# Optimization experiments

Measured on AMD Instinct MI355X. Metric: run time of the kernel, lower is better.

## Reference

```python
import jax, jax.numpy as jnp
import numpy as np

D_MODEL = 1024
NUM_HEADS = 16
HEAD_DIM = D_MODEL // NUM_HEADS
FF_DIM = 4096
EPS = 1e-5


def _layer_norm(x, gamma, beta):
    mu = jnp.mean(x, axis=-1, keepdims=True)
    var = jnp.var(x, axis=-1, keepdims=True)
    return (x - mu) * jax.lax.rsqrt(var + EPS) * gamma + beta


def setup_inputs() -> dict:
    key0 = jax.random.key(0)
    ks = jax.random.split(key0, 20)
    s = 0.02
    B, S = 2, 2048
    inp = {
        'value': jax.random.normal(ks[0], (B, S, D_MODEL), jnp.float32),
        'key': jax.random.normal(ks[1], (B, S, D_MODEL), jnp.float32),
        'query': jax.random.normal(ks[2], (B, S, D_MODEL), jnp.float32),
        # attention projections (stored [in, out]; y = x @ W + b)
        'wq': jax.random.normal(ks[3], (D_MODEL, D_MODEL), jnp.float32) * s,
        'bq': jnp.zeros((D_MODEL,), jnp.float32),
        'wk': jax.random.normal(ks[4], (D_MODEL, D_MODEL), jnp.float32) * s,
        'bk': jnp.zeros((D_MODEL,), jnp.float32),
        'wv': jax.random.normal(ks[5], (D_MODEL, D_MODEL), jnp.float32) * s,
        'bv': jnp.zeros((D_MODEL,), jnp.float32),
        'wo': jax.random.normal(ks[6], (D_MODEL, D_MODEL), jnp.float32) * s,
        'bo': jnp.zeros((D_MODEL,), jnp.float32),
        # layernorm 1
        'g1': jnp.ones((D_MODEL,), jnp.float32),
        'beta1': jnp.zeros((D_MODEL,), jnp.float32),
        # feed-forward
        'w1': jax.random.normal(ks[7], (D_MODEL, FF_DIM), jnp.float32) * s,
        'b1': jnp.zeros((FF_DIM,), jnp.float32),
        'w2': jax.random.normal(ks[8], (FF_DIM, D_MODEL), jnp.float32) * s,
        'b2': jnp.zeros((D_MODEL,), jnp.float32),
        # layernorm 2
        'g2': jnp.ones((D_MODEL,), jnp.float32),
        'beta2': jnp.zeros((D_MODEL,), jnp.float32),
    }
    return inp


def reference(value, key, query, wq, bq, wk, bk, wv, bv, wo, bo,
              g1, beta1, w1, b1, w2, b2, g2, beta2):
    B, S, _ = query.shape
    # QKV projections -> [B, S, H, Dh]
    Q = (query @ wq + bq).reshape(B, S, NUM_HEADS, HEAD_DIM)
    K = (key @ wk + bk).reshape(B, S, NUM_HEADS, HEAD_DIM)
    V = (value @ wv + bv).reshape(B, S, NUM_HEADS, HEAD_DIM)
    # scaled dot-product attention (full score matrix, as in source)
    energy = jnp.einsum('bqhd,bkhd->bhqk', Q, K) / jnp.sqrt(jnp.float32(HEAD_DIM))
    attn = jax.nn.softmax(energy, axis=-1)
    out = jnp.einsum('bhqk,bkhd->bqhd', attn, V).reshape(B, S, D_MODEL)
    attn_out = out @ wo + bo
    # residual + norm1 (dropout is identity in eval)
    x = _layer_norm(attn_out + query, g1, beta1)
    # feed-forward
    ff = jax.nn.relu(x @ w1 + b1) @ w2 + b2
    # residual + norm2
    return _layer_norm(ff + x, g2, beta2)
```

## Files before the change

kernel.cpp:

```cpp
#include <hip/hip_runtime.h>
#include <hip/hip_bf16.h>
#include <cstdint>
#include <math.h>

typedef __bf16 bf16_t;
typedef __attribute__((ext_vector_type(2))) __bf16 bf16x2;
typedef __attribute__((ext_vector_type(4))) __bf16 bf16x4;
typedef __attribute__((ext_vector_type(8))) __bf16 bf16x8;
typedef __attribute__((ext_vector_type(4))) float f32x4;
typedef __attribute__((ext_vector_type(16))) float f32x16;
typedef __attribute__((ext_vector_type(2))) int int2v;
typedef __attribute__((ext_vector_type(4))) int int4v;

#define B_SZ 2
#define S_SZ 2048
#define D_MODEL 1024
#define NUM_HEADS 16
#define HEAD_DIM 64
#define FF_DIM 4096
#define M_ROWS (B_SZ * S_SZ)

#define CF 0.180336880f
#define THRC 2.0f

__device__ __forceinline__ float fexp2(float x) { return __builtin_amdgcn_exp2f(x); }

__device__ __forceinline__ void gload_lds16(const void* g, void* lds) {
    __builtin_amdgcn_global_load_lds(
        (const __attribute__((address_space(1))) void*)(uintptr_t)g,
        (__attribute__((address_space(3))) void*)(uint32_t)(uintptr_t)lds,
        16, 0, 0);
}

__device__ __forceinline__ f32x4 mfma16(bf16x8 a, bf16x8 b, f32x4 c) {
    return __builtin_amdgcn_mfma_f32_16x16x32_bf16(a, b, c, 0, 0, 0);
}
__device__ __forceinline__ f32x16 mfma32(bf16x8 a, bf16x8 b, f32x16 c) {
    return __builtin_amdgcn_mfma_f32_32x32x16_bf16(a, b, c, 0, 0, 0);
}
__device__ __forceinline__ int2v plswap(int a, int b) {
    return __builtin_amdgcn_permlane32_swap(a, b, false, false);
}
__device__ __forceinline__ int packbf(float a, float b) {
    bf16x2 t; t[0] = (bf16_t)a; t[1] = (bf16_t)b;
    return __builtin_bit_cast(int, t);
}

__device__ __forceinline__ int xcd_swz(int lin, int nwg) {
    return (lin & 7) * (nwg >> 3) + (lin >> 3);
}

__global__ __launch_bounds__(256) void cast3_f32_bf16(const float* __restrict__ in0,
                                                      const float* __restrict__ in1,
                                                      const float* __restrict__ in2,
                                                      bf16_t* __restrict__ out0,
                                                      bf16_t* __restrict__ out1,
                                                      bf16_t* __restrict__ out2) {
    int which = blockIdx.x >> 12;
    int blk = blockIdx.x & 4095;
    const float* in = which == 0 ? in0 : which == 1 ? in1 : in2;
    bf16_t* out = which == 0 ? out0 : which == 1 ? out1 : out2;
    size_t i = ((size_t)blk * 256 + threadIdx.x) * 4;
    float4 v = *(const float4*)(in + i);
    bf16x4 o;
    o[0] = (bf16_t)v.x; o[1] = (bf16_t)v.y; o[2] = (bf16_t)v.z; o[3] = (bf16_t)v.w;
    *(bf16x4*)(out + i) = o;
}

__global__ __launch_bounds__(256) void transpose_cast_w4(const float* __restrict__ W0,
                                                         const float* __restrict__ W1,
                                                         const float* __restrict__ W2,
                                                         const float* __restrict__ W3,
                                                         bf16_t* __restrict__ T0,
                                                         bf16_t* __restrict__ T1,
                                                         bf16_t* __restrict__ T2,
                                                         bf16_t* __restrict__ T3) {
    __shared__ float t[32][33];
    const int K = 1024, N = 1024;
    const float* W = blockIdx.z == 0 ? W0 : blockIdx.z == 1 ? W1 : blockIdx.z == 2 ? W2 : W3;
    bf16_t* WT = blockIdx.z == 0 ? T0 : blockIdx.z == 1 ? T1 : blockIdx.z == 2 ? T2 : T3;
    int tid = threadIdx.x;
    int rr = tid >> 3, cc = (tid & 7) * 4;
    int k0 = blockIdx.x * 32, n0 = blockIdx.y * 32;
    float4 v = *(const float4*)(W + (size_t)(k0 + rr) * N + n0 + cc);
    t[rr][cc + 0] = v.x; t[rr][cc + 1] = v.y; t[rr][cc + 2] = v.z; t[rr][cc + 3] = v.w;
    __syncthreads();
    bf16x4 o;
    o[0] = (bf16_t)t[cc + 0][rr]; o[1] = (bf16_t)t[cc + 1][rr];
    o[2] = (bf16_t)t[cc + 2][rr]; o[3] = (bf16_t)t[cc + 3][rr];
    *(bf16x4*)(WT + (size_t)(n0 + rr) * K + k0 + cc) = o;
}

__global__ __launch_bounds__(256) void transpose_cast_w(const float* __restrict__ W,
                                                        bf16_t* __restrict__ WT,
                                                        int K, int N) {
    __shared__ float t[32][33];
    int tid = threadIdx.x;
    int rr = tid >> 3, cc = (tid & 7) * 4;
    int k0 = blockIdx.x * 32, n0 = blockIdx.y * 32;
    float4 v = *(const float4*)(W + (size_t)(k0 + rr) * N + n0 + cc);
    t[rr][cc + 0] = v.x; t[rr][cc + 1] = v.y; t[rr][cc + 2] = v.z; t[rr][cc + 3] = v.w;
    __syncthreads();
    bf16x4 o;
    o[0] = (bf16_t)t[cc + 0][rr]; o[1] = (bf16_t)t[cc + 1][rr];
    o[2] = (bf16_t)t[cc + 2][rr]; o[3] = (bf16_t)t[cc + 3][rr];
    *(bf16x4*)(WT + (size_t)(n0 + rr) * K + k0 + cc) = o;
}

__global__ __launch_bounds__(256) void transpose_v(const bf16_t* __restrict__ Vp,
                                                   bf16_t* __restrict__ VT) {
    __shared__ bf16_t t[32][34];
    int tid = threadIdx.x;
    int rr = tid >> 3, cc = (tid & 7) * 4;
    int bh = blockIdx.z;
    int b = bh >> 4, h = bh & 15;
    int s0 = blockIdx.x * 32, d0 = blockIdx.y * 32;
    bf16x4 v = *(const bf16x4*)(Vp + ((size_t)(b * S_SZ + s0 + rr)) * D_MODEL + h * HEAD_DIM + d0 + cc);
    t[rr][cc + 0] = v[0]; t[rr][cc + 1] = v[1]; t[rr][cc + 2] = v[2]; t[rr][cc + 3] = v[3];
    __syncthreads();
    bf16x4 o;
    o[0] = t[cc + 0][rr]; o[1] = t[cc + 1][rr]; o[2] = t[cc + 2][rr]; o[3] = t[cc + 3][rr];
    *(bf16x4*)(VT + ((size_t)(bh * HEAD_DIM + d0 + rr)) * S_SZ + s0 + cc) = o;
}

template<int BNF, bool RELU, bool OUT_BF16, bool OUT_F32>
__device__ __forceinline__ void gemm8p_core(const bf16_t* __restrict__ Ag, int lda,
                                            const bf16_t* __restrict__ Bg, int ldb,
                                            const float* __restrict__ bias, bool useBias,
                                            float* __restrict__ Cf,
                                            bf16_t* __restrict__ Cb,
                                            int N, int Klen, int m0, int n0,
                                            bf16_t* sA, bf16_t* sB) {
    constexpr int BSTRIDE = (BNF == 4) ? 16384 : 8192;
    const int tid = threadIdx.x;
    const int lane = tid & 63, w = tid >> 6;
    const int g = lane >> 4, r = lane & 15;
    const int ah = w >> 2;
    const int bh = (BNF == 4) ? ((w & 3) >> 1) : 0;
    const int wbr = (BNF == 4) ? ((w & 1) * 64) : ((w & 3) * 32);
    const int rs = r & 7;

    const int scol = ((tid & 7) ^ ((tid >> 3) & 7)) * 8;
    const bf16_t* aSrc = Ag + (size_t)(m0 + (tid >> 3)) * lda + scol;
    const bf16_t* bSrc = Bg + (size_t)(n0 + (tid >> 3)) * ldb + scol;

    f32x4 acc[8][BNF];
#pragma unroll
    for (int i = 0; i < 8; i++)
#pragma unroll
        for (int j = 0; j < BNF; j++)
#pragma unroll
            for (int e = 0; e < 4; e++) acc[i][j][e] = 0.f;

    auto stageA = [&](int buf, int half, int k0) {
        const bf16_t* s = aSrc + (size_t)(half * 128) * lda + k0;
        bf16_t* d = sA + buf * 16384 + half * 8192 + tid * 8;
        gload_lds16(s, d);
        gload_lds16(s + (size_t)64 * lda, d + 4096);
    };
    auto stageB = [&](int buf, int half, int k0) {
        const bf16_t* s = bSrc + (size_t)(half * 128) * ldb + k0;
        bf16_t* d = sB + buf * BSTRIDE + half * 8192 + tid * 8;
        gload_lds16(s, d);
        gload_lds16(s + (size_t)64 * ldb, d + 4096);
    };

    bf16x8 af[4][2];
    bf16x8 bfr[BNF / 2][2];

    auto READ = [&](int buf, int ih, int jsel) {
        const bf16_t* mA = sA + buf * 16384 + ah * 8192;
        const bf16_t* mB = sB + buf * BSTRIDE + bh * 8192;
#pragma unroll
        for (int ii = 0; ii < 4; ii++) {
            const int rho = ih + ii * 16 + r;
#pragma unroll
            for (int kk = 0; kk < 2; kk++)
                af[ii][kk] = *(const bf16x8*)(mA + rho * 64 + (((kk << 2) | g) ^ rs) * 8);
        }
#pragma unroll
        for (int jj = 0; jj < BNF / 2; jj++) {
            const int rho = wbr + jsel * (BNF == 4 ? 32 : 16) + jj * 16 + r;
#pragma unroll
            for (int kk = 0; kk < 2; kk++)
                bfr[jj][kk] = *(const bf16x8*)(mB + rho * 64 + (((kk << 2) | g) ^ rs) * 8);
        }
    };
    auto QUAD = [&](int ih4, int jsel) {
        __builtin_amdgcn_s_setprio(1);
#pragma unroll
        for (int ii = 0; ii < 4; ii++)
#pragma unroll
            for (int jj = 0; jj < BNF / 2; jj++)
#pragma unroll
                for (int kk = 0; kk < 2; kk++)
                    acc[ih4 + ii][jsel * (BNF / 2) + jj] =
                        mfma16(af[ii][kk], bfr[jj][kk], acc[ih4 + ii][jsel * (BNF / 2) + jj]);
        __builtin_amdgcn_s_setprio(0);
    };

#define LGKM0() do { asm volatile("s_waitcnt lgkmcnt(0)" ::: "memory"); \
                     __builtin_amdgcn_sched_barrier(0); } while (0)

    const int nk = Klen >> 6;
    stageA(0, 0, 0); stageA(0, 1, 0); stageB(0, 0, 0);
    if constexpr (BNF == 4) stageB(0, 1, 0);

    for (int t = 0; t < nk; ++t) {
        const int buf = t & 1, nb = buf ^ 1;
        const int kn = (t + 1) << 6;
        const bool hn = (t + 1 < nk);
        if (hn) { stageA(nb, 0, kn); asm volatile("s_waitcnt vmcnt(2)" ::: "memory"); }
        else    { asm volatile("s_waitcnt vmcnt(0)" ::: "memory"); }
        __builtin_amdgcn_s_barrier();
        READ(buf, 0, 0);
        LGKM0();
        QUAD(0, 0);
        __builtin_amdgcn_s_barrier();
        READ(buf, 0, 1);
        if (hn) stageA(nb, 1, kn);
        __builtin_amdgcn_s_barrier();
        LGKM0();
        QUAD(0, 1);
        __builtin_amdgcn_s_barrier();
        READ(buf, 64, 0);
        if (hn) stageB(nb, 0, kn);
        __builtin_amdgcn_s_barrier();
        LGKM0();
        QUAD(4, 0);
        __builtin_amdgcn_s_barrier();
        READ(buf, 64, 1);
        if constexpr (BNF == 4) { if (hn) stageB(nb, 1, kn); }
        __builtin_amdgcn_s_barrier();
        LGKM0();
        QUAD(4, 1);
        __builtin_amdgcn_s_barrier();
    }
#undef LGKM0

#pragma unroll
    for (int j = 0; j < BNF; j++) {
        int n = n0 + (w & 3) * (16 * BNF) + j * 16 + r;
        float bv = useBias ? bias[n] : 0.f;
#pragma unroll
        for (int i = 0; i < 8; i++) {
#pragma unroll
            for (int rr = 0; rr < 4; rr++) {
                int mrow = m0 + (w >> 2) * 128 + i * 16 + g * 4 + rr;
                float val = acc[i][j][rr] + bv;
                if (RELU) val = fmaxf(val, 0.f);
                if (OUT_F32) Cf[(size_t)mrow * N + n] = val;
                if (OUT_BF16) Cb[(size_t)mrow * N + n] = (bf16_t)val;
            }
        }
    }
}

template<int BNF, bool RELU, bool OUT_BF16, bool OUT_F32>
__global__ __launch_bounds__(512, 1) void gemm8p(const bf16_t* __restrict__ A, int lda,
                                                 const bf16_t* __restrict__ Bt, int ldb,
                                                 const float* __restrict__ bias,
                                                 float* __restrict__ Cf0,
                                                 float* __restrict__ Cf1,
                                                 bf16_t* __restrict__ Cb,
                                                 int N, int Klen) {
    __shared__ bf16_t sA[2 * 16384];
    __shared__ bf16_t sB[2 * ((BNF == 4) ? 16384 : 8192)];
    const int lin = blockIdx.x + gridDim.x * (blockIdx.y + gridDim.y * blockIdx.z);
    const int nwg = gridDim.x * gridDim.y * gridDim.z;
    const int sz = xcd_swz(lin, nwg);
    const int bx = sz % gridDim.x;
    const int rest = sz / gridDim.x;
    const int by = rest % gridDim.y;
    const int bz = rest / gridDim.y;
    const int koff = bz * Klen;
    gemm8p_core<BNF, RELU, OUT_BF16, OUT_F32>(A + koff, lda, Bt + koff, ldb,
                                              bias, bz == 0,
                                              bz ? Cf1 : Cf0, Cb, N, Klen,
                                              bx * 256, by * (64 * BNF), sA, sB);
}

__global__ __launch_bounds__(512, 1) void gemm_qkv8p(const bf16_t* __restrict__ A0,
                                                     const bf16_t* __restrict__ A1,
                                                     const bf16_t* __restrict__ A2,
                                                     const bf16_t* __restrict__ B0,
                                                     const bf16_t* __restrict__ B1,
                                                     const bf16_t* __restrict__ B2,
                                                     const float* __restrict__ b0,
                                                     const float* __restrict__ b1,
                                                     const float* __restrict__ b2,
                                                     bf16_t* __restrict__ C0,
                                                     bf16_t* __restrict__ C1,
                                                     bf16_t* __restrict__ C2) {
    __shared__ bf16_t sA[2 * 16384];
    __shared__ bf16_t sB[2 * 16384];
    const int lin = blockIdx.x + gridDim.x * (blockIdx.y + gridDim.y * blockIdx.z);
    const int nwg = gridDim.x * gridDim.y * gridDim.z;
    const int sz = xcd_swz(lin, nwg);
    const int bx = sz % gridDim.x;
    const int rest = sz / gridDim.x;
    const int by = rest % gridDim.y;
    const int bz = rest / gridDim.y;
    const bf16_t* A = bz == 0 ? A0 : bz == 1 ? A1 : A2;
    const bf16_t* Bt = bz == 0 ? B0 : bz == 1 ? B1 : B2;
    const float* bias = bz == 0 ? b0 : bz == 1 ? b1 : b2;
    bf16_t* C = bz == 0 ? C0 : bz == 1 ? C1 : C2;
    gemm8p_core<4, false, true, false>(A, 1024, Bt, 1024, bias, true,
                                       nullptr, C, 1024, 1024, bx * 256, by * 256, sA, sB);
}

__device__ __forceinline__ void flash_tile(
    const char* kt, const char* vt, int l31, int hi,
    const bf16x8 (&bq)[4],
    f32x16& o0, f32x16& o1, float& mC, float& l_run)
{
    bf16x8 ak[4];
#pragma unroll
    for (int kb = 0; kb < 4; kb++)
        ak[kb] = *(const bf16x8*)(kt + l31 * 128 + (((kb << 1) | hi) ^ (l31 & 7)) * 16);
    bf16x8 av[4];
#pragma unroll
    for (int db = 0; db < 2; db++)
#pragma unroll
        for (int kb = 0; kb < 2; kb++)
            av[db * 2 + kb] = *(const bf16x8*)(vt + (db * 32 + l31) * 64 + ((((kb << 1) | hi)) ^ ((l31 >> 1) & 3)) * 16);

    f32x16 s;
#pragma unroll
    for (int e = 0; e < 16; e++) s[e] = 0.f;
#pragma unroll
    for (int kb = 0; kb < 4; kb++) s = mfma32(ak[kb], bq[kb], s);

    float ma = fmaxf(fmaxf(s[0], s[1]), fmaxf(s[2], s[3]));
    float mb = fmaxf(fmaxf(s[4], s[5]), fmaxf(s[6], s[7]));
    float mc = fmaxf(fmaxf(s[8], s[9]), fmaxf(s[10], s[11]));
    float md = fmaxf(fmaxf(s[12], s[13]), fmaxf(s[14], s[15]));
    float pmaxC = fmaxf(fmaxf(ma, mb), fmaxf(mc, md)) * CF;

    if (!__all(pmaxC <= mC + THRC)) {
        int2v pr = plswap(__float_as_int(pmaxC), __float_as_int(pmaxC));
        float rowmaxC = fmaxf(__int_as_float(pr[0]), __int_as_float(pr[1]));
        float mnewC = fmaxf(mC, rowmaxC);
        float alpha = fexp2(mC - mnewC);
        mC = mnewC;
        l_run *= alpha;
#pragma unroll
        for (int e = 0; e < 16; e++) { o0[e] *= alpha; o1[e] *= alpha; }
    }

#pragma unroll
    for (int e = 0; e < 16; e++) s[e] = fexp2(__builtin_fmaf(s[e], CF, -mC));
    float t0 = (s[0] + s[1]) + (s[2] + s[3]);
    float t1 = (s[4] + s[5]) + (s[6] + s[7]);
    float t2 = (s[8] + s[9]) + (s[10] + s[11]);
    float t3 = (s[12] + s[13]) + (s[14] + s[15]);
    l_run += (t0 + t1) + (t2 + t3);

#pragma unroll
    for (int kb2 = 0; kb2 < 2; kb2++) {
        const int bse = kb2 * 8;
        int W0 = packbf(s[bse + 0], s[bse + 1]);
        int W1 = packbf(s[bse + 2], s[bse + 3]);
        int W2 = packbf(s[bse + 4], s[bse + 5]);
        int W3 = packbf(s[bse + 6], s[bse + 7]);
        int2v r02 = plswap(W0, W2);
        int2v r13 = plswap(W1, W3);
        int4v fw; fw[0] = r02[0]; fw[1] = r13[0]; fw[2] = r02[1]; fw[3] = r13[1];
        bf16x8 pf = __builtin_bit_cast(bf16x8, fw);
        o0 = mfma32(av[kb2], pf, o0);
        o1 = mfma32(av[2 + kb2], pf, o1);
    }
}

__global__ __launch_bounds__(256) void flash_attn(const bf16_t* __restrict__ Qp,
                                                  const bf16_t* __restrict__ Kp,
                                                  const bf16_t* __restrict__ VT,
                                                  bf16_t* __restrict__ Oa) {
    __shared__ alignas(16) char lds[2][2][8192];
    const int tid = threadIdx.x;
    const int lane = tid & 63;
    const int wave = tid >> 6;
    const int half = wave >> 1;
    const int qt = wave & 1;
    const int l31 = lane & 31, hi = lane >> 5;

    const int lin = blockIdx.x + (blockIdx.y << 5) + (blockIdx.z << 9);
    const int swz = (lin & 7) * 128 + (lin >> 3);
    const int qb = swz & 31;
    const int h = (swz >> 5) & 15;
    const int b = swz >> 9;

    const int q0 = qb * 64 + qt * 32;

    const bf16_t* Qb = Qp + (size_t)b * S_SZ * D_MODEL + h * HEAD_DIM;
    const bf16_t* Kb = Kp + (size_t)b * S_SZ * D_MODEL + h * HEAD_DIM;
    const bf16_t* Vb = VT + ((size_t)(b * NUM_HEADS + h) * HEAD_DIM) * S_SZ;

    const int sh = wave & 1;
    const int skvbase = sh * (S_SZ / 2);
    const bool kRole = wave < 2;

    const bf16_t* src_run;
    size_t inner_stride;
    size_t tile_stride;
    char* dst0;
    char* dst1;
    if (kRole) {
        src_run = Kb + (size_t)(skvbase + (lane >> 3)) * D_MODEL + ((lane & 7) ^ (lane >> 3)) * 8;
        inner_stride = (size_t)8 * D_MODEL;
        tile_stride = (size_t)32 * D_MODEL;
        dst0 = &lds[0][sh][0] + lane * 16;
        dst1 = &lds[1][sh][0] + lane * 16;
    } else {
        src_run = Vb + (size_t)(lane >> 2) * S_SZ + skvbase + ((lane & 3) ^ ((lane >> 3) & 3)) * 8;
        inner_stride = (size_t)16 * S_SZ;
        tile_stride = 32;
        dst0 = &lds[0][sh][4096] + lane * 16;
        dst1 = &lds[1][sh][4096] + lane * 16;
    }

    bf16x8 bq[4];
#pragma unroll
    for (int kb = 0; kb < 4; kb++)
        bq[kb] = *(const bf16x8*)(Qb + (size_t)(q0 + l31) * D_MODEL + kb * 16 + hi * 8);

    f32x16 o0, o1;
#pragma unroll
    for (int e = 0; e < 16; e++) { o0[e] = 0.f; o1[e] = 0.f; }
    float mC = -1e30f, l_run = 0.f;

    const char* kt0 = &lds[0][half][0];
    const char* vt0 = &lds[0][half][4096];
    const char* kt1 = &lds[1][half][0];
    const char* vt1 = &lds[1][half][4096];

#pragma unroll
    for (int ii = 0; ii < 4; ii++)
        gload_lds16(src_run + ii * inner_stride, dst0 + ii * 1024);
    src_run += tile_stride;
    __syncthreads();

    for (int t = 0; t < 32; t += 2) {
#pragma unroll
        for (int ii = 0; ii < 4; ii++)
            gload_lds16(src_run + ii * inner_stride, dst1 + ii * 1024);
        src_run += tile_stride;
        flash_tile(kt0, vt0, l31, hi, bq, o0, o1, mC, l_run);
        __syncthreads();

        if (t + 2 < 32) {
#pragma unroll
            for (int ii = 0; ii < 4; ii++)
                gload_lds16(src_run + ii * inner_stride, dst0 + ii * 1024);
            src_run += tile_stride;
        }
        flash_tile(kt1, vt1, l31, hi, bq, o0, o1, mC, l_run);
        __syncthreads();
    }

    int2v lp = plswap(__float_as_int(l_run), __float_as_int(l_run));
    l_run = __int_as_float(lp[0]) + __int_as_float(lp[1]);

    float (*obuf)[2][64] = (float (*)[2][64])(&lds[0][0][0]);
    float (*mrg)[64][2] = (float (*)[64][2])(&lds[0][0][0] + 16384);
    if (half == 1) {
        mrg[qt][lane][0] = mC;
        mrg[qt][lane][1] = l_run;
#pragma unroll
        for (int e = 0; e < 16; e++) {
            obuf[e][qt][lane] = o0[e];
            obuf[16 + e][qt][lane] = o1[e];
        }
    }
    __syncthreads();
    if (half == 0) {
        const float m2C = mrg[qt][lane][0], l2 = mrg[qt][lane][1];
        const float mm = fmaxf(mC, m2C);
        const float e1 = fexp2(mC - mm);
        const float e2 = fexp2(m2C - mm);
        const float linv = 1.f / (l_run * e1 + l2 * e2);
        bf16_t* Orow = Oa + ((size_t)b * S_SZ + q0 + l31) * D_MODEL + h * HEAD_DIM;
#pragma unroll
        for (int db = 0; db < 2; db++) {
#pragma unroll
            for (int rq = 0; rq < 4; rq++) {
                bf16x4 st;
#pragma unroll
                for (int i = 0; i < 4; i++) {
                    const int e = rq * 4 + i;
                    const float own = db ? o1[e] : o0[e];
                    const float oth = obuf[db * 16 + e][qt][lane];
                    st[i] = (bf16_t)((own * e1 + oth * e2) * linv);
                }
                *(bf16x4*)(Orow + db * 32 + rq * 8 + hi * 4) = st;
            }
        }
    }
}

__global__ __launch_bounds__(256) void ln_fused(const float* __restrict__ A,
                                                const float* __restrict__ A2,
                                                const float* __restrict__ R,
                                                const float* __restrict__ gamma,
                                                const float* __restrict__ beta,
                                                float* __restrict__ Xf,
                                                bf16_t* __restrict__ Xb) {
    __shared__ float red[8];
    int row = blockIdx.x, tid = threadIdx.x;
    size_t base = (size_t)row * D_MODEL + tid * 4;
    float4 a = *(const float4*)(A + base);
    float4 rv = *(const float4*)(R + base);
    float v0 = a.x + rv.x, v1 = a.y + rv.y, v2 = a.z + rv.z, v3 = a.w + rv.w;
    if (A2) {
        float4 a2 = *(const float4*)(A2 + base);
        v0 += a2.x; v1 += a2.y; v2 += a2.z; v3 += a2.w;
    }
    float s = v0 + v1 + v2 + v3;
    float q = v0 * v0 + v1 * v1 + v2 * v2 + v3 * v3;
#pragma unroll
    for (int off = 32; off; off >>= 1) { s += __shfl_down(s, off); q += __shfl_down(q, off); }
    if ((tid & 63) == 0) { red[tid >> 6] = s; red[4 + (tid >> 6)] = q; }
    __syncthreads();
    s = red[0] + red[1] + red[2] + red[3];
    q = red[4] + red[5] + red[6] + red[7];
    float mean = s * (1.f / D_MODEL);
    float var = q * (1.f / D_MODEL) - mean * mean;
    float rstd = rsqrtf(var + 1e-5f);
    float4 gm = *(const float4*)(gamma + tid * 4);
    float4 bt = *(const float4*)(beta + tid * 4);
    float y0 = (v0 - mean) * rstd * gm.x + bt.x;
    float y1 = (v1 - mean) * rstd * gm.y + bt.y;
    float y2 = (v2 - mean) * rstd * gm.z + bt.z;
    float y3 = (v3 - mean) * rstd * gm.w + bt.w;
    float4 yo; yo.x = y0; yo.y = y1; yo.z = y2; yo.w = y3;
    *(float4*)(Xf + base) = yo;
    if (Xb) {
        bf16x4 ob; ob[0] = (bf16_t)y0; ob[1] = (bf16_t)y1; ob[2] = (bf16_t)y2; ob[3] = (bf16_t)y3;
        *(bf16x4*)(Xb + base) = ob;
    }
}

extern "C" void kernel_launch(void* const* d_in, const int* in_sizes, int n_in,
                              void* d_out, int out_size, void* d_ws, size_t ws_size,
                              hipStream_t stream) {
    const float* value = (const float*)d_in[0];
    const float* key   = (const float*)d_in[1];
    const float* query = (const float*)d_in[2];
    const float* wq = (const float*)d_in[3];
    const float* bq = (const float*)d_in[4];
    const float* wk = (const float*)d_in[5];
    const float* bk = (const float*)d_in[6];
    const float* wv = (const float*)d_in[7];
    const float* bv = (const float*)d_in[8];
    const float* wo = (const float*)d_in[9];
    const float* bo = (const float*)d_in[10];
    const float* g1 = (const float*)d_in[11];
    const float* beta1 = (const float*)d_in[12];
    const float* w1 = (const float*)d_in[13];
    const float* b1 = (const float*)d_in[14];
    const float* w2 = (const float*)d_in[15];
    const float* b2 = (const float*)d_in[16];
    const float* g2 = (const float*)d_in[17];
    const float* beta2 = (const float*)d_in[18];
    (void)in_sizes; (void)n_in; (void)out_size; (void)ws_size;

    const size_t MB = 1ull << 20;
    char* ws = (char*)d_ws;
    bf16_t* wqT = (bf16_t*)(ws + 0 * MB);
    bf16_t* wkT = (bf16_t*)(ws + 2 * MB);
    bf16_t* wvT = (bf16_t*)(ws + 4 * MB);
    bf16_t* woT = (bf16_t*)(ws + 6 * MB);
    bf16_t* w1T = (bf16_t*)(ws + 8 * MB);
    bf16_t* w2T = (bf16_t*)(ws + 16 * MB);
    bf16_t* q_bf = (bf16_t*)(ws + 24 * MB);
    bf16_t* k_bf = (bf16_t*)(ws + 32 * MB);
    bf16_t* v_bf = (bf16_t*)(ws + 40 * MB);
    bf16_t* Qp  = (bf16_t*)(ws + 48 * MB);
    bf16_t* Kp  = (bf16_t*)(ws + 56 * MB);
    bf16_t* Vp  = (bf16_t*)(ws + 64 * MB);
    bf16_t* VT  = (bf16_t*)(ws + 72 * MB);
    bf16_t* attn = (bf16_t*)(ws + 24 * MB);
    float*  woP0 = (float*)(ws + 32 * MB);
    float*  woP1 = (float*)(ws + 48 * MB);
    float*  x_f = (float*)(ws + 64 * MB);
    bf16_t* x_b = (bf16_t*)(ws + 24 * MB);
    bf16_t* h_b = (bf16_t*)(ws + 32 * MB);
    float*  ffP0 = (float*)(ws + 80 * MB);
    float*  ffP1 = (float*)(ws + 96 * MB);

    dim3 blk(256);
    dim3 blk512(512);

    cast3_f32_bf16<<<12288, blk, 0, stream>>>(query, key, value, q_bf, k_bf, v_bf);
    transpose_cast_w4<<<dim3(32, 32, 4), blk, 0, stream>>>(wq, wk, wv, wo, wqT, wkT, wvT, woT);
    transpose_cast_w<<<dim3(32, 128), blk, 0, stream>>>(w1, w1T, 1024, 4096);
    transpose_cast_w<<<dim3(128, 32), blk, 0, stream>>>(w2, w2T, 4096, 1024);

    gemm_qkv8p<<<dim3(16, 4, 3), blk512, 0, stream>>>(q_bf, k_bf, v_bf, wqT, wkT, wvT,
                                                      bq, bk, bv, Qp, Kp, Vp);

    transpose_v<<<dim3(64, 2, 32), blk, 0, stream>>>(Vp, VT);

    flash_attn<<<dim3(32, 16, 2), blk, 0, stream>>>(Qp, Kp, VT, attn);

    gemm8p<2, false, false, true><<<dim3(16, 8, 2), blk512, 0, stream>>>(attn, 1024, woT, 1024, bo, woP0, woP1, nullptr, D_MODEL, 512);

    ln_fused<<<4096, blk, 0, stream>>>(woP0, woP1, query, g1, beta1, x_f, x_b);

    gemm8p<4, true, true, false><<<dim3(16, 16, 1), blk512, 0, stream>>>(x_b, 1024, w1T, 1024, b1, nullptr, nullptr, h_b, FF_DIM, 1024);

    gemm8p<2, false, false, true><<<dim3(16, 8, 2), blk512, 0, stream>>>(h_b, 4096, w2T, 4096, b2, ffP0, ffP1, nullptr, D_MODEL, 2048);

    ln_fused<<<4096, blk, 0, stream>>>(ffP0, ffP1, x_f, g2, beta2, (float*)d_out, nullptr);
}
```

Before: 266.2 us.

## Switch GEMM core from 16x16 to 32x32 MFMA tiles with new LDS pipeline

Rewrites the shared GEMM core to use 32x32x16 bf16 MFMA instructions with f32x16 accumulators instead of 16x16 tiles. Each warp now owns a 128 x 32*NJT output block, reading one k-slice per step in four steps per 64-wide K tile. The global-to-LDS staging is re-split into quarter loads spread over those steps. A full vmcnt(0) wait at the end of each iteration replaces the partial waits. The larger MFMA shape cuts LDS read traffic and instruction count per FLOP, at the cost of a different register footprint and a less overlapped prefetch.

```diff
diff --git a/kernel.cpp b/kernel.cpp
--- a/kernel.cpp
+++ b/kernel.cpp
@@ -123,7 +123,7 @@
     *(bf16x4*)(VT + ((size_t)(bh * HEAD_DIM + d0 + rr)) * S_SZ + s0 + cc) = o;
 }
 
-template<int BNF, bool RELU, bool OUT_BF16, bool OUT_F32>
+template<int NJT, bool RELU, bool OUT_BF16, bool OUT_F32>
 __device__ __forceinline__ void gemm8p_core(const bf16_t* __restrict__ Ag, int lda,
                                             const bf16_t* __restrict__ Bg, int ldb,
                                             const float* __restrict__ bias, bool useBias,
@@ -131,71 +131,53 @@
                                             bf16_t* __restrict__ Cb,
                                             int N, int Klen, int m0, int n0,
                                             bf16_t* sA, bf16_t* sB) {
-    constexpr int BSTRIDE = (BNF == 4) ? 16384 : 8192;
+    constexpr int BELE = 8192 * NJT;
+    constexpr int NBQ = 2 * NJT;
     const int tid = threadIdx.x;
     const int lane = tid & 63, w = tid >> 6;
-    const int g = lane >> 4, r = lane & 15;
-    const int ah = w >> 2;
-    const int bh = (BNF == 4) ? ((w & 3) >> 1) : 0;
-    const int wbr = (BNF == 4) ? ((w & 1) * 64) : ((w & 3) * 32);
-    const int rs = r & 7;
+    const int l31 = lane & 31, hi = lane >> 5;
+    const int wm = (w >> 2) * 128;
+    const int wn = (w & 3) * (32 * NJT);
+    const int rs7 = l31 & 7;
 
     const int scol = ((tid & 7) ^ ((tid >> 3) & 7)) * 8;
     const bf16_t* aSrc = Ag + (size_t)(m0 + (tid >> 3)) * lda + scol;
     const bf16_t* bSrc = Bg + (size_t)(n0 + (tid >> 3)) * ldb + scol;
 
-    f32x4 acc[8][BNF];
-#pragma unroll
-    for (int i = 0; i < 8; i++)
-#pragma unroll
-        for (int j = 0; j < BNF; j++)
-#pragma unroll
-            for (int e = 0; e < 4; e++) acc[i][j][e] = 0.f;
-
-    auto stageA = [&](int buf, int half, int k0) {
-        const bf16_t* s = aSrc + (size_t)(half * 128) * lda + k0;
-        bf16_t* d = sA + buf * 16384 + half * 8192 + tid * 8;
-        gload_lds16(s, d);
-        gload_lds16(s + (size_t)64 * lda, d + 4096);
+    f32x16 acc[4][NJT];
+#pragma unroll
+    for (int it = 0; it < 4; it++)
+#pragma unroll
+        for (int jt = 0; jt < NJT; jt++)
+#pragma unroll
+            for (int e = 0; e < 16; e++) acc[it][jt][e] = 0.f;
+
+    auto stA = [&](int buf, int q, int k0) {
+        gload_lds16(aSrc + (size_t)(q * 64) * lda + k0, sA + buf * 16384 + q * 4096 + tid * 8);
     };
-    auto stageB = [&](int buf, int half, int k0) {
-        const bf16_t* s = bSrc + (size_t)(half * 128) * ldb + k0;
-        bf16_t* d = sB + buf * BSTRIDE + half * 8192 + tid * 8;
-        gload_lds16(s, d);
-        gload_lds16(s + (size_t)64 * ldb, d + 4096);
+    auto stB = [&](int buf, int q, int k0) {
+        gload_lds16(bSrc + (size_t)(q * 64) * ldb + k0, sB + buf * BELE + q * 4096 + tid * 8);
     };
 
-    bf16x8 af[4][2];
-    bf16x8 bfr[BNF / 2][2];
-
-    auto READ = [&](int buf, int ih, int jsel) {
-        const bf16_t* mA = sA + buf * 16384 + ah * 8192;
-        const bf16_t* mB = sB + buf * BSTRIDE + bh * 8192;
-#pragma unroll
-        for (int ii = 0; ii < 4; ii++) {
-            const int rho = ih + ii * 16 + r;
-#pragma unroll
-            for (int kk = 0; kk < 2; kk++)
-                af[ii][kk] = *(const bf16x8*)(mA + rho * 64 + (((kk << 2) | g) ^ rs) * 8);
-        }
-#pragma unroll
-        for (int jj = 0; jj < BNF / 2; jj++) {
-            const int rho = wbr + jsel * (BNF == 4 ? 32 : 16) + jj * 16 + r;
-#pragma unroll
-            for (int kk = 0; kk < 2; kk++)
-                bfr[jj][kk] = *(const bf16x8*)(mB + rho * 64 + (((kk << 2) | g) ^ rs) * 8);
-        }
+    bf16x8 a[4], b[NJT];
+    auto RD = [&](int buf, int ks) {
+        const bf16_t* bA = sA + buf * 16384;
+        const bf16_t* bB = sB + buf * BELE;
+        const int cs = ((((ks << 1) | hi)) ^ rs7) << 3;
+#pragma unroll
+        for (int it = 0; it < 4; it++)
+            a[it] = *(const bf16x8*)(bA + (wm + it * 32 + l31) * 64 + cs);
+#pragma unroll
+        for (int jt = 0; jt < NJT; jt++)
+            b[jt] = *(const bf16x8*)(bB + (wn + jt * 32 + l31) * 64 + cs);
     };
-    auto QUAD = [&](int ih4, int jsel) {
+    auto MM = [&]() {
         __builtin_amdgcn_s_setprio(1);
 #pragma unroll
-        for (int ii = 0; ii < 4; ii++)
-#pragma unroll
-            for (int jj = 0; jj < BNF / 2; jj++)
-#pragma unroll
-                for (int kk = 0; kk < 2; kk++)
-                    acc[ih4 + ii][jsel * (BNF / 2) + jj] =
-                        mfma16(af[ii][kk], bfr[jj][kk], acc[ih4 + ii][jsel * (BNF / 2) + jj]);
+        for (int it = 0; it < 4; it++)
+#pragma unroll
+            for (int jt = 0; jt < NJT; jt++)
+                acc[it][jt] = mfma32(a[it], b[jt], acc[it][jt]);
         __builtin_amdgcn_s_setprio(0);
     };
 
@@ -203,51 +185,54 @@
                      __builtin_amdgcn_sched_barrier(0); } while (0)
 
     const int nk = Klen >> 6;
-    stageA(0, 0, 0); stageA(0, 1, 0); stageB(0, 0, 0);
-    if constexpr (BNF == 4) stageB(0, 1, 0);
+#pragma unroll
+    for (int q = 0; q < 4; q++) stA(0, q, 0);
+#pragma unroll
+    for (int q = 0; q < NBQ; q++) stB(0, q, 0);
+    asm volatile("s_waitcnt vmcnt(0)" ::: "memory");
+    __builtin_amdgcn_s_barrier();
 
     for (int t = 0; t < nk; ++t) {
         const int buf = t & 1, nb = buf ^ 1;
         const int kn = (t + 1) << 6;
         const bool hn = (t + 1 < nk);
-        if (hn) { stageA(nb, 0, kn); asm volatile("s_waitcnt vmcnt(2)" ::: "memory"); }
-        else    { asm volatile("s_waitcnt vmcnt(0)" ::: "memory"); }
-        __builtin_amdgcn_s_barrier();
-        READ(buf, 0, 0);
+        RD(buf, 0);
+        if (hn) { stA(nb, 0, kn); stA(nb, 1, kn); stA(nb, 2, kn); }
+        __builtin_amdgcn_s_barrier();
         LGKM0();
-        QUAD(0, 0);
-        __builtin_amdgcn_s_barrier();
-        READ(buf, 0, 1);
-        if (hn) stageA(nb, 1, kn);
+        MM();
+        __builtin_amdgcn_s_barrier();
+        RD(buf, 1);
+        if (hn) { stA(nb, 3, kn); stB(nb, 0, kn); if (NBQ > 1) stB(nb, 1, kn); }
         __builtin_amdgcn_s_barrier();
         LGKM0();
-        QUAD(0, 1);
-        __builtin_amdgcn_s_barrier();
-        READ(buf, 64, 0);
-        if (hn) stageB(nb, 0, kn);
+        MM();
+        __builtin_amdgcn_s_barrier();
+        RD(buf, 2);
+        if (hn && NBQ > 2) { stB(nb, 2, kn); stB(nb, 3, kn); }
         __builtin_amdgcn_s_barrier();
         LGKM0();
-        QUAD(4, 0);
-        __builtin_amdgcn_s_barrier();
-        READ(buf, 64, 1);
-        if constexpr (BNF == 4) { if (hn) stageB(nb, 1, kn); }
+        MM();
+        __builtin_amdgcn_s_barrier();
+        RD(buf, 3);
         __builtin_amdgcn_s_barrier();
         LGKM0();
-        QUAD(4, 1);
+        MM();
+        asm volatile("s_waitcnt vmcnt(0)" ::: "memory");
         __builtin_amdgcn_s_barrier();
     }
 #undef LGKM0
 
 #pragma unroll
-    for (int j = 0; j < BNF; j++) {
-        int n = n0 + (w & 3) * (16 * BNF) + j * 16 + r;
-        float bv = useBias ? bias[n] : 0.f;
-#pragma unroll
-        for (int i = 0; i < 8; i++) {
-#pragma unroll
-            for (int rr = 0; rr < 4; rr++) {
-                int mrow = m0 + (w >> 2) * 128 + i * 16 + g * 4 + rr;
-                float val = acc[i][j][rr] + bv;
+    for (int it = 0; it < 4; it++) {
+#pragma unroll
+        for (int jt = 0; jt < NJT; jt++) {
+            const int n = n0 + wn + jt * 32 + l31;
+            const float bv = useBias ? bias[n] : 0.f;
+#pragma unroll
+            for (int e = 0; e < 16; e++) {
+                const int mrow = m0 + wm + it * 32 + (e & 3) + ((e >> 2) << 3) + hi * 4;
+                float val = acc[it][jt][e] + bv;
                 if (RELU) val = fmaxf(val, 0.f);
                 if (OUT_F32) Cf[(size_t)mrow * N + n] = val;
                 if (OUT_BF16) Cb[(size_t)mrow * N + n] = (bf16_t)val;
@@ -256,7 +241,7 @@
     }
 }
 
-template<int BNF, bool RELU, bool OUT_BF16, bool OUT_F32>
+template<int NJT, bool RELU, bool OUT_BF16, bool OUT_F32>
 __global__ __launch_bounds__(512, 1) void gemm8p(const bf16_t* __restrict__ A, int lda,
                                                  const bf16_t* __restrict__ Bt, int ldb,
                                                  const float* __restrict__ bias,
@@ -265,7 +250,7 @@
                                                  bf16_t* __restrict__ Cb,
                                                  int N, int Klen) {
     __shared__ bf16_t sA[2 * 16384];
-    __shared__ bf16_t sB[2 * ((BNF == 4) ? 16384 : 8192)];
+    __shared__ bf16_t sB[2 * 8192 * NJT];
     const int lin = blockIdx.x + gridDim.x * (blockIdx.y + gridDim.y * blockIdx.z);
     const int nwg = gridDim.x * gridDim.y * gridDim.z;
     const int sz = xcd_swz(lin, nwg);
@@ -274,10 +259,10 @@
     const int by = rest % gridDim.y;
     const int bz = rest / gridDim.y;
     const int koff = bz * Klen;
-    gemm8p_core<BNF, RELU, OUT_BF16, OUT_F32>(A + koff, lda, Bt + koff, ldb,
+    gemm8p_core<NJT, RELU, OUT_BF16, OUT_F32>(A + koff, lda, Bt + koff, ldb,
                                               bias, bz == 0,
                                               bz ? Cf1 : Cf0, Cb, N, Klen,
-                                              bx * 256, by * (64 * BNF), sA, sB);
+                                              bx * 256, by * (128 * NJT), sA, sB);
 }
 
 __global__ __launch_bounds__(512, 1) void gemm_qkv8p(const bf16_t* __restrict__ A0,
@@ -305,7 +290,7 @@
     const bf16_t* Bt = bz == 0 ? B0 : bz == 1 ? B1 : B2;
     const float* bias = bz == 0 ? b0 : bz == 1 ? b1 : b2;
     bf16_t* C = bz == 0 ? C0 : bz == 1 ? C1 : C2;
-    gemm8p_core<4, false, true, false>(A, 1024, Bt, 1024, bias, true,
+    gemm8p_core<2, false, true, false>(A, 1024, Bt, 1024, bias, true,
                                        nullptr, C, 1024, 1024, bx * 256, by * 256, sA, sB);
 }
 
@@ -603,13 +588,13 @@
 
     flash_attn<<<dim3(32, 16, 2), blk, 0, stream>>>(Qp, Kp, VT, attn);
 
-    gemm8p<2, false, false, true><<<dim3(16, 8, 2), blk512, 0, stream>>>(attn, 1024, woT, 1024, bo, woP0, woP1, nullptr, D_MODEL, 512);
+    gemm8p<1, false, false, true><<<dim3(16, 8, 2), blk512, 0, stream>>>(attn, 1024, woT, 1024, bo, woP0, woP1, nullptr, D_MODEL, 512);
 
     ln_fused<<<4096, blk, 0, stream>>>(woP0, woP1, query, g1, beta1, x_f, x_b);
 
-    gemm8p<4, true, true, false><<<dim3(16, 16, 1), blk512, 0, stream>>>(x_b, 1024, w1T, 1024, b1, nullptr, nullptr, h_b, FF_DIM, 1024);
-
-    gemm8p<2, false, false, true><<<dim3(16, 8, 2), blk512, 0, stream>>>(h_b, 4096, w2T, 4096, b2, ffP0, ffP1, nullptr, D_MODEL, 2048);
+    gemm8p<2, true, true, false><<<dim3(16, 16, 1), blk512, 0, stream>>>(x_b, 1024, w1T, 1024, b1, nullptr, nullptr, h_b, FF_DIM, 1024);
+
+    gemm8p<1, false, false, true><<<dim3(16, 8, 2), blk512, 0, stream>>>(h_b, 4096, w2T, 4096, b2, ffP0, ffP1, nullptr, D_MODEL, 2048);
 
     ln_fused<<<4096, blk, 0, stream>>>(ffP0, ffP1, x_f, g2, beta2, (float*)d_out, nullptr);
 }
```

After: 249.2 us. -6.4%, faster.
